# Kernel tuning notes

Measured on AMD Instinct MI355X. Metric: run time of the kernel, lower is better.

## Reference

```python
import jax, jax.numpy as jnp
import numpy as np

N = 50000      # nodes
E = 800000     # edges
D = 128        # hidden_dim == out_dim
VOCAB = 50000  # in_size


def setup_inputs() -> dict:
    key = jax.random.key(0)
    ks = jax.random.split(key, 8)
    batch = jax.random.randint(ks[0], (N,), 0, VOCAB)
    src = jax.random.randint(ks[1], (E,), 0, N)
    dst = jax.random.randint(ks[2], (E,), 0, N)
    emb = jax.random.normal(ks[3], (VOCAB, D), dtype=jnp.float32) * 0.02
    s = 1.0 / np.sqrt(D)
    W1 = jax.random.normal(ks[4], (D, D), dtype=jnp.float32) * s
    W2 = jax.random.normal(ks[5], (D, D), dtype=jnp.float32) * s
    W3 = jax.random.normal(ks[6], (D, D), dtype=jnp.float32) * s
    b1 = jnp.zeros((D,), jnp.float32)
    b2 = jnp.zeros((D,), jnp.float32)
    b3 = jnp.zeros((D,), jnp.float32)
    return {"batch": batch, "src": src, "dst": dst, "emb": emb,
            "W1": W1, "b1": b1, "W2": W2, "b2": b2, "W3": W3, "b3": b3}


def reference(batch, src, dst, emb, W1, b1, W2, b2, W3, b3):
    # embedding lookup over node ids
    x = emb[batch]  # [N, D]
    ones = jnp.ones((E,), x.dtype)
    # DGL GraphConv norm='both': symmetric normalization, degrees clamped >= 1
    deg_out = jnp.clip(jax.ops.segment_sum(ones, src, num_segments=N), 1.0)
    deg_in = jnp.clip(jax.ops.segment_sum(ones, dst, num_segments=N), 1.0)
    norm_src = deg_out ** -0.5  # [N]
    norm_dst = deg_in ** -0.5   # [N]

    def gcn_layer(h, W, b):
        m = (h * norm_src[:, None])[src]                       # gather src messages [E, D]
        agg = jax.ops.segment_sum(m, dst, num_segments=N)      # SpMM aggregate [N, D]
        agg = agg * norm_dst[:, None]
        # dropout p=0.0 is identity; activation is ReLU
        return jax.nn.relu(agg @ W + b)

    x = gcn_layer(x, W1, b1)
    x = gcn_layer(x, W2, b2)
    x = gcn_layer(x, W3, b3)
    return x
```

## Files before the change

### kernel.cpp

```cpp
#include <hip/hip_runtime.h>
#include <math.h>

typedef float f4 __attribute__((ext_vector_type(4)));
typedef float f32x4 __attribute__((ext_vector_type(4)));
typedef short s8 __attribute__((ext_vector_type(8)));
typedef short s4 __attribute__((ext_vector_type(4)));

static constexpr int N = 50000;
static constexpr int E = 800000;
static constexpr int D = 128;
static constexpr int SCAN_NB = (N + 255) / 256;
static constexpr int MBLK = 128;
static constexpr int GRID_M = (N + MBLK - 1) / MBLK;
static constexpr int N_PAD = GRID_M * MBLK;
static constexpr int WT_PITCH = 136;

__device__ inline unsigned short f32_bf16_rne(float x) {
    unsigned u = __float_as_uint(x);
    return (unsigned short)((u + 0x7FFF + ((u >> 16) & 1)) >> 16);
}
__device__ inline float bf16_f32(unsigned short h) {
    return __uint_as_float((unsigned)h << 16);
}

__global__ void deg_kernel(const int* __restrict__ src, const int* __restrict__ dst,
                           int* __restrict__ deg_out, int* __restrict__ deg_in) {
    int e = blockIdx.x * 256 + threadIdx.x;
    if (e < E) {
        atomicAdd(&deg_out[src[e]], 1);
        atomicAdd(&deg_in[dst[e]], 1);
    }
}

__global__ __launch_bounds__(256) void scan_bsum_norm_kernel(
    const int* __restrict__ deg_out, const int* __restrict__ deg_in,
    float* __restrict__ norm_src, float* __restrict__ norm_dst,
    int* __restrict__ bsums) {
    int i = blockIdx.x * 256 + threadIdx.x;
    int v = 0;
    if (i < N) {
        norm_src[i] = rsqrtf(fmaxf((float)deg_out[i], 1.0f));
        norm_dst[i] = rsqrtf(fmaxf((float)deg_in[i], 1.0f));
        v = deg_in[i];
    }
#pragma unroll
    for (int off = 1; off < 64; off <<= 1) v += __shfl_xor(v, off, 64);
    __shared__ int ws[4];
    if ((threadIdx.x & 63) == 0) ws[threadIdx.x >> 6] = v;
    __syncthreads();
    if (threadIdx.x == 0) bsums[blockIdx.x] = ws[0] + ws[1] + ws[2] + ws[3];
}

__global__ __launch_bounds__(256) void scan_final_kernel(const int* __restrict__ deg,
                                                         const int* __restrict__ bsums,
                                                         int* __restrict__ row_ptr) {
    __shared__ int s[256];
    __shared__ int base_s;
    int b = blockIdx.x, t = threadIdx.x;

    int bv = (t < b && t < SCAN_NB) ? bsums[t] : 0;
#pragma unroll
    for (int off = 1; off < 64; off <<= 1) bv += __shfl_xor(bv, off, 64);
    __shared__ int wsb[4];
    if ((t & 63) == 0) wsb[t >> 6] = bv;
    __syncthreads();
    if (t == 0) base_s = wsb[0] + wsb[1] + wsb[2] + wsb[3];

    int i = b * 256 + t;
    s[t] = (i < N) ? deg[i] : 0;
    __syncthreads();
    for (int off = 1; off < 256; off <<= 1) {
        int v = (t >= off) ? s[t - off] : 0;
        __syncthreads();
        s[t] += v;
        __syncthreads();
    }
    if (i < N) row_ptr[i + 1] = s[t] + base_s;
    if (i == 0) row_ptr[0] = 0;
}

__global__ void fill_kernel(const int* __restrict__ src, const int* __restrict__ dst,
                            const int* __restrict__ row_ptr, int* __restrict__ cursor,
                            unsigned short* __restrict__ csr_src) {
    int e = blockIdx.x * 256 + threadIdx.x;
    if (e < E) {
        int d = dst[e];
        int pos = row_ptr[d] + atomicAdd(&cursor[d], 1);
        csr_src[pos] = (unsigned short)src[e];
    }
}

__global__ void gather_kernel(const int* __restrict__ batch, const float* __restrict__ emb,
                              const float* __restrict__ norm_src, float* __restrict__ hs) {
    int gid = blockIdx.x * 256 + threadIdx.x;
    int i = gid >> 5;
    int c = (gid & 31) << 2;
    if (i < N) {
        float s = norm_src[i];
        f4 v = *(const f4*)(emb + (size_t)batch[i] * D + c);
        *(f4*)(hs + (size_t)i * D + c) = v * s;
    }
}

__global__ void agg_kernel(const int* __restrict__ row_ptr,
                           const unsigned short* __restrict__ csr_src,
                           const float* __restrict__ hs,
                           short* __restrict__ agg_h, short* __restrict__ agg_l) {
    int gid = blockIdx.x * 256 + threadIdx.x;
    int node = gid >> 6;
    if (node >= N) return;
    int lane = threadIdx.x & 63;
    int grp = lane >> 5;
    int col = (lane & 31) << 2;
    int beg = row_ptr[node], end = row_ptr[node + 1];

    f4 a0 = (f4)0.0f, a1 = (f4)0.0f, a2 = (f4)0.0f, a3 = (f4)0.0f;
    f4 a4 = (f4)0.0f, a5 = (f4)0.0f, a6 = (f4)0.0f, a7 = (f4)0.0f;
    int e = beg + grp;
    for (; e + 14 < end; e += 16) {
        int s0 = csr_src[e];
        int s1 = csr_src[e + 2];
        int s2 = csr_src[e + 4];
        int s3 = csr_src[e + 6];
        int s4 = csr_src[e + 8];
        int s5 = csr_src[e + 10];
        int s6 = csr_src[e + 12];
        int s7 = csr_src[e + 14];
        a0 += *(const f4*)(hs + (size_t)s0 * D + col);
        a1 += *(const f4*)(hs + (size_t)s1 * D + col);
        a2 += *(const f4*)(hs + (size_t)s2 * D + col);
        a3 += *(const f4*)(hs + (size_t)s3 * D + col);
        a4 += *(const f4*)(hs + (size_t)s4 * D + col);
        a5 += *(const f4*)(hs + (size_t)s5 * D + col);
        a6 += *(const f4*)(hs + (size_t)s6 * D + col);
        a7 += *(const f4*)(hs + (size_t)s7 * D + col);
    }
    for (; e < end; e += 2)
        a0 += *(const f4*)(hs + (size_t)csr_src[e] * D + col);
    a0 += a1; a2 += a3; a4 += a5; a6 += a7;
    a0 += a2; a4 += a6;
    a0 += a4;

    f4 o;
#pragma unroll
    for (int j = 0; j < 4; ++j)
        o[j] = a0[j] + __shfl_xor(a0[j], 32, 64);
    if (grp == 0) {
        s4 oh, ol;
#pragma unroll
        for (int j = 0; j < 4; ++j) {
            unsigned short h = f32_bf16_rne(o[j]);
            oh[j] = (short)h;
            ol[j] = (short)f32_bf16_rne(o[j] - bf16_f32(h));
        }
        *(s4*)(agg_h + (size_t)node * D + col) = oh;
        *(s4*)(agg_l + (size_t)node * D + col) = ol;
    }
}

__global__ void wprep_kernel(const float* __restrict__ W1, const float* __restrict__ W2,
                             const float* __restrict__ W3, short* __restrict__ wt) {
    int idx = blockIdx.x * 256 + threadIdx.x;
    if (idx >= 3 * D * D) return;
    int l = idx >> 14;
    int e = idx & (D * D - 1);
    int n = e >> 7, k = e & 127;
    const float* W = (l == 0) ? W1 : ((l == 1) ? W2 : W3);
    float w = W[(size_t)k * D + n];
    unsigned short h = f32_bf16_rne(w);
    unsigned short lo = f32_bf16_rne(w - bf16_f32(h));
    wt[(size_t)l * 2 * D * D + (size_t)n * D + k] = (short)h;
    wt[(size_t)l * 2 * D * D + D * D + (size_t)n * D + k] = (short)lo;
}

__global__ __launch_bounds__(512, 2) void gemm_mfma_kernel(
    const short* __restrict__ Ah, const short* __restrict__ Al,
    const short* __restrict__ wth,
    const float* __restrict__ bias, const float* __restrict__ norm_dst,
    const float* __restrict__ post, float* __restrict__ out) {
    __shared__ short wt_h[D * WT_PITCH];
    __shared__ short wt_l[D * WT_PITCH];

    int tid = threadIdx.x;
    const short* gh = wth;
    const short* gl = wth + (size_t)D * D;

#pragma unroll
    for (int it = 0; it < 4; ++it) {
        int c = tid + it * 512;
        int n = c >> 4, kc = c & 15;
        *(s8*)(&wt_h[n * WT_PITCH + kc * 8]) = *(const s8*)(gh + (size_t)n * D + kc * 8);
        *(s8*)(&wt_l[n * WT_PITCH + kc * 8]) = *(const s8*)(gl + (size_t)n * D + kc * 8);
    }
    __syncthreads();

    int wv = tid >> 6;
    int lane = tid & 63;
    int lg = lane >> 4;
    int lr = lane & 15;

    int arow = blockIdx.x * MBLK + wv * 16 + lr;
    const short* ahp = Ah + (size_t)arow * D;
    const short* alp = Al + (size_t)arow * D;

    f32x4 acc[8];
#pragma unroll
    for (int nt = 0; nt < 8; ++nt) acc[nt] = (f32x4)0.0f;

#pragma unroll
    for (int kt = 0; kt < 4; ++kt) {
        int ko = kt * 32 + lg * 8;
        s8 ah = *(const s8*)(ahp + ko);
        s8 al = *(const s8*)(alp + ko);
#pragma unroll
        for (int nt = 0; nt < 8; ++nt) {
            int bidx = (nt * 16 + lr) * WT_PITCH + ko;
            s8 bh = *(const s8*)(&wt_h[bidx]);
            s8 bl = *(const s8*)(&wt_l[bidx]);
            acc[nt] = __builtin_amdgcn_mfma_f32_16x16x32_bf16(ah, bh, acc[nt], 0, 0, 0);
            acc[nt] = __builtin_amdgcn_mfma_f32_16x16x32_bf16(al, bh, acc[nt], 0, 0, 0);
            acc[nt] = __builtin_amdgcn_mfma_f32_16x16x32_bf16(ah, bl, acc[nt], 0, 0, 0);
        }
    }

    int r0 = blockIdx.x * MBLK + wv * 16 + lg * 4;
    float nd[4], ps[4];
#pragma unroll
    for (int i = 0; i < 4; ++i) {
        int gr = r0 + i;
        nd[i] = (gr < N) ? norm_dst[gr] : 0.0f;
        ps[i] = (gr < N) ? (post ? post[gr] : 1.0f) : 0.0f;
    }
#pragma unroll
    for (int nt = 0; nt < 8; ++nt) {
        int col = nt * 16 + lr;
        float bv = bias[col];
#pragma unroll
        for (int i = 0; i < 4; ++i) {
            int gr = r0 + i;
            if (gr < N) {
                float v = fmaxf(acc[nt][i] * nd[i] + bv, 0.0f) * ps[i];
                out[(size_t)gr * D + col] = v;
            }
        }
    }
}

extern "C" void kernel_launch(void* const* d_in, const int* in_sizes, int n_in,
                              void* d_out, int out_size, void* d_ws, size_t ws_size,
                              hipStream_t stream) {
    const int*   batch = (const int*)d_in[0];
    const int*   src   = (const int*)d_in[1];
    const int*   dst   = (const int*)d_in[2];
    const float* emb   = (const float*)d_in[3];
    const float* W1    = (const float*)d_in[4];
    const float* b1    = (const float*)d_in[5];
    const float* W2    = (const float*)d_in[6];
    const float* b2    = (const float*)d_in[7];
    const float* W3    = (const float*)d_in[8];
    const float* b3    = (const float*)d_in[9];
    float* out = (float*)d_out;

    float*          norm_src = (float*)d_ws;
    float*          norm_dst = norm_src + N;
    int*            row_ptr  = (int*)(norm_dst + N);
    unsigned short* csr_src  = (unsigned short*)(row_ptr + (N + 1));
    float*          hs       = (float*)(csr_src + E) + 2;
    short*          agg_h    = (short*)(hs + (size_t)N_PAD * D);
    short*          agg_l    = agg_h + (size_t)N_PAD * D;
    short*          wt       = agg_l + (size_t)N_PAD * D;
    int*            deg_out  = (int*)agg_h;
    int*            deg_in   = deg_out + N;
    int*            cursor   = deg_in + N;
    int*            bsums    = cursor + N;

    hipMemsetAsync(deg_out, 0, 3 * (size_t)N * sizeof(int), stream);
    deg_kernel<<<(E + 255) / 256, 256, 0, stream>>>(src, dst, deg_out, deg_in);
    scan_bsum_norm_kernel<<<SCAN_NB, 256, 0, stream>>>(deg_out, deg_in,
                                                       norm_src, norm_dst, bsums);
    scan_final_kernel<<<SCAN_NB, 256, 0, stream>>>(deg_in, bsums, row_ptr);
    fill_kernel<<<(E + 255) / 256, 256, 0, stream>>>(src, dst, row_ptr, cursor,
                                                     csr_src);
    gather_kernel<<<((size_t)N * 32 + 255) / 256, 256, 0, stream>>>(batch, emb,
                                                                    norm_src, hs);
    wprep_kernel<<<(3 * D * D + 255) / 256, 256, 0, stream>>>(W1, W2, W3, wt);

    const float* bs[3] = {b1, b2, b3};
    for (int l = 0; l < 3; ++l) {
        bool last = (l == 2);
        agg_kernel<<<((size_t)N * 64 + 255) / 256, 256, 0, stream>>>(
            row_ptr, csr_src, hs, agg_h, agg_l);
        gemm_mfma_kernel<<<GRID_M, 512, 0, stream>>>(
            agg_h, agg_l, wt + (size_t)l * 2 * D * D, bs[l], norm_dst,
            last ? nullptr : norm_src,
            last ? out : hs);
    }
}
```

Before: 378.1 us.

## Slice features into column blocks and aggregate per slice with XCC-affine work queues

Stores node features and aggregated outputs in 16 column slices of 8 floats each, so every gather for a slice reads from a 1.6MB working set that can stay in cache. The aggregation kernel becomes persistent: blocks pull 256-node chunks from per-slice atomic queues, and each XCC starts on a different slice to improve L2 locality. Each thread now handles a whole node for one slice, which replaces the wavefront-per-node scheme. The cost is 16 passes over the CSR indices, load imbalance between threads that have different degrees, and a GEMM that now reads A and writes hs in the strided slice layout.

```diff
diff --git a/kernel.cpp b/kernel.cpp
--- a/kernel.cpp
+++ b/kernel.cpp
@@ -1,10 +1,10 @@
 #include <hip/hip_runtime.h>
 #include <math.h>
+#include <stdint.h>
 
 typedef float f4 __attribute__((ext_vector_type(4)));
 typedef float f32x4 __attribute__((ext_vector_type(4)));
 typedef short s8 __attribute__((ext_vector_type(8)));
-typedef short s4 __attribute__((ext_vector_type(4)));
 
 static constexpr int N = 50000;
 static constexpr int E = 800000;
@@ -14,6 +14,10 @@
 static constexpr int GRID_M = (N + MBLK - 1) / MBLK;
 static constexpr int N_PAD = GRID_M * MBLK;
 static constexpr int WT_PITCH = 136;
+static constexpr int NSLICE = 16;
+static constexpr size_t SL = (size_t)N_PAD * 8;
+static constexpr int AGG_BLOCKS = 1024;
+static constexpr int CHUNK = 256;
 
 __device__ inline unsigned short f32_bf16_rne(float x) {
     unsigned u = __float_as_uint(x);
@@ -91,70 +95,15 @@
 }
 
 __global__ void gather_kernel(const int* __restrict__ batch, const float* __restrict__ emb,
-                              const float* __restrict__ norm_src, float* __restrict__ hs) {
+                              const float* __restrict__ norm_src, float* __restrict__ hs_t) {
     int gid = blockIdx.x * 256 + threadIdx.x;
     int i = gid >> 5;
     int c = (gid & 31) << 2;
     if (i < N) {
         float s = norm_src[i];
         f4 v = *(const f4*)(emb + (size_t)batch[i] * D + c);
-        *(f4*)(hs + (size_t)i * D + c) = v * s;
-    }
-}
-
-__global__ void agg_kernel(const int* __restrict__ row_ptr,
-                           const unsigned short* __restrict__ csr_src,
-                           const float* __restrict__ hs,
-                           short* __restrict__ agg_h, short* __restrict__ agg_l) {
-    int gid = blockIdx.x * 256 + threadIdx.x;
-    int node = gid >> 6;
-    if (node >= N) return;
-    int lane = threadIdx.x & 63;
-    int grp = lane >> 5;
-    int col = (lane & 31) << 2;
-    int beg = row_ptr[node], end = row_ptr[node + 1];
-
-    f4 a0 = (f4)0.0f, a1 = (f4)0.0f, a2 = (f4)0.0f, a3 = (f4)0.0f;
-    f4 a4 = (f4)0.0f, a5 = (f4)0.0f, a6 = (f4)0.0f, a7 = (f4)0.0f;
-    int e = beg + grp;
-    for (; e + 14 < end; e += 16) {
-        int s0 = csr_src[e];
-        int s1 = csr_src[e + 2];
-        int s2 = csr_src[e + 4];
-        int s3 = csr_src[e + 6];
-        int s4 = csr_src[e + 8];
-        int s5 = csr_src[e + 10];
-        int s6 = csr_src[e + 12];
-        int s7 = csr_src[e + 14];
-        a0 += *(const f4*)(hs + (size_t)s0 * D + col);
-        a1 += *(const f4*)(hs + (size_t)s1 * D + col);
-        a2 += *(const f4*)(hs + (size_t)s2 * D + col);
-        a3 += *(const f4*)(hs + (size_t)s3 * D + col);
-        a4 += *(const f4*)(hs + (size_t)s4 * D + col);
-        a5 += *(const f4*)(hs + (size_t)s5 * D + col);
-        a6 += *(const f4*)(hs + (size_t)s6 * D + col);
-        a7 += *(const f4*)(hs + (size_t)s7 * D + col);
-    }
-    for (; e < end; e += 2)
-        a0 += *(const f4*)(hs + (size_t)csr_src[e] * D + col);
-    a0 += a1; a2 += a3; a4 += a5; a6 += a7;
-    a0 += a2; a4 += a6;
-    a0 += a4;
-
-    f4 o;
-#pragma unroll
-    for (int j = 0; j < 4; ++j)
-        o[j] = a0[j] + __shfl_xor(a0[j], 32, 64);
-    if (grp == 0) {
-        s4 oh, ol;
-#pragma unroll
-        for (int j = 0; j < 4; ++j) {
-            unsigned short h = f32_bf16_rne(o[j]);
-            oh[j] = (short)h;
-            ol[j] = (short)f32_bf16_rne(o[j] - bf16_f32(h));
-        }
-        *(s4*)(agg_h + (size_t)node * D + col) = oh;
-        *(s4*)(agg_l + (size_t)node * D + col) = ol;
+        int slice = c >> 3, cc = c & 7;
+        *(f4*)(hs_t + (size_t)slice * SL + (size_t)i * 8 + cc) = v * s;
     }
 }
 
@@ -173,6 +122,71 @@
     wt[(size_t)l * 2 * D * D + D * D + (size_t)n * D + k] = (short)lo;
 }
 
+__global__ __launch_bounds__(256) void agg_kernel(
+    const int* __restrict__ row_ptr, const unsigned short* __restrict__ csr_src,
+    const float* __restrict__ hs_t,
+    short* __restrict__ agg_h_t, short* __restrict__ agg_l_t,
+    int* __restrict__ qcur) {
+    unsigned xcc;
+    asm volatile("s_getreg_b32 %0, hwreg(HW_REG_XCC_ID)" : "=s"(xcc));
+    int tid = threadIdx.x;
+    __shared__ int chunk_s;
+
+    for (int qi = 0; qi < NSLICE; ++qi) {
+        int q = ((xcc << 1) + qi) & (NSLICE - 1);
+        const float* hsq = hs_t + (size_t)q * SL;
+        short* ahq = agg_h_t + (size_t)q * SL;
+        short* alq = agg_l_t + (size_t)q * SL;
+        while (true) {
+            __syncthreads();
+            if (tid == 0) chunk_s = atomicAdd(&qcur[q], CHUNK);
+            __syncthreads();
+            int base = chunk_s;
+            if (base >= N) break;
+            int node = base + tid;
+            if (node < N) {
+                int beg = row_ptr[node], end = row_ptr[node + 1];
+                f4 a0 = (f4)0.0f, a1 = (f4)0.0f, a2 = (f4)0.0f, a3 = (f4)0.0f;
+                f4 b0 = (f4)0.0f, b1 = (f4)0.0f, b2 = (f4)0.0f, b3 = (f4)0.0f;
+                int e = beg;
+                for (; e + 3 < end; e += 4) {
+                    int s0 = csr_src[e];
+                    int s1 = csr_src[e + 1];
+                    int s2 = csr_src[e + 2];
+                    int s3 = csr_src[e + 3];
+                    const f4* p0 = (const f4*)(hsq + (size_t)s0 * 8);
+                    const f4* p1 = (const f4*)(hsq + (size_t)s1 * 8);
+                    const f4* p2 = (const f4*)(hsq + (size_t)s2 * 8);
+                    const f4* p3 = (const f4*)(hsq + (size_t)s3 * 8);
+                    a0 += p0[0]; b0 += p0[1];
+                    a1 += p1[0]; b1 += p1[1];
+                    a2 += p2[0]; b2 += p2[1];
+                    a3 += p3[0]; b3 += p3[1];
+                }
+                for (; e < end; ++e) {
+                    const f4* p0 = (const f4*)(hsq + (size_t)csr_src[e] * 8);
+                    a0 += p0[0]; b0 += p0[1];
+                }
+                a0 += a1; a2 += a3; a0 += a2;
+                b0 += b1; b2 += b3; b0 += b2;
+
+                s8 oh, ol;
+#pragma unroll
+                for (int j = 0; j < 4; ++j) {
+                    unsigned short h = f32_bf16_rne(a0[j]);
+                    oh[j] = (short)h;
+                    ol[j] = (short)f32_bf16_rne(a0[j] - bf16_f32(h));
+                    unsigned short h2 = f32_bf16_rne(b0[j]);
+                    oh[j + 4] = (short)h2;
+                    ol[j + 4] = (short)f32_bf16_rne(b0[j] - bf16_f32(h2));
+                }
+                *(s8*)(ahq + (size_t)node * 8) = oh;
+                *(s8*)(alq + (size_t)node * 8) = ol;
+            }
+        }
+    }
+}
+
 __global__ __launch_bounds__(512, 2) void gemm_mfma_kernel(
     const short* __restrict__ Ah, const short* __restrict__ Al,
     const short* __restrict__ wth,
@@ -200,8 +214,6 @@
     int lr = lane & 15;
 
     int arow = blockIdx.x * MBLK + wv * 16 + lr;
-    const short* ahp = Ah + (size_t)arow * D;
-    const short* alp = Al + (size_t)arow * D;
 
     f32x4 acc[8];
 #pragma unroll
@@ -209,9 +221,10 @@
 
 #pragma unroll
     for (int kt = 0; kt < 4; ++kt) {
+        int slice = kt * 4 + lg;
+        s8 ah = *(const s8*)(Ah + (size_t)slice * SL + (size_t)arow * 8);
+        s8 al = *(const s8*)(Al + (size_t)slice * SL + (size_t)arow * 8);
         int ko = kt * 32 + lg * 8;
-        s8 ah = *(const s8*)(ahp + ko);
-        s8 al = *(const s8*)(alp + ko);
 #pragma unroll
         for (int nt = 0; nt < 8; ++nt) {
             int bidx = (nt * 16 + lr) * WT_PITCH + ko;
@@ -240,7 +253,12 @@
             int gr = r0 + i;
             if (gr < N) {
                 float v = fmaxf(acc[nt][i] * nd[i] + bv, 0.0f) * ps[i];
-                out[(size_t)gr * D + col] = v;
+                if (post) {
+                    int slice = col >> 3, cc = col & 7;
+                    out[(size_t)slice * SL + (size_t)gr * 8 + cc] = v;
+                } else {
+                    out[(size_t)gr * D + col] = v;
+                }
             }
         }
     }
@@ -265,16 +283,18 @@
     float*          norm_dst = norm_src + N;
     int*            row_ptr  = (int*)(norm_dst + N);
     unsigned short* csr_src  = (unsigned short*)(row_ptr + (N + 1));
-    float*          hs       = (float*)(csr_src + E) + 2;
-    short*          agg_h    = (short*)(hs + (size_t)N_PAD * D);
-    short*          agg_l    = agg_h + (size_t)N_PAD * D;
-    short*          wt       = agg_l + (size_t)N_PAD * D;
-    int*            deg_out  = (int*)agg_h;
+    float*          hs_t     = (float*)((((uintptr_t)(csr_src + E)) + 15) & ~(uintptr_t)15);
+    short*          agg_h_t  = (short*)(hs_t + (size_t)NSLICE * SL);
+    short*          agg_l_t  = agg_h_t + (size_t)NSLICE * SL;
+    short*          wt       = agg_l_t + (size_t)NSLICE * SL;
+    int*            qcur     = (int*)(wt + (size_t)3 * 2 * D * D);
+    int*            deg_out  = (int*)agg_h_t;
     int*            deg_in   = deg_out + N;
     int*            cursor   = deg_in + N;
     int*            bsums    = cursor + N;
 
     hipMemsetAsync(deg_out, 0, 3 * (size_t)N * sizeof(int), stream);
+    hipMemsetAsync(qcur, 0, 3 * NSLICE * sizeof(int), stream);
     deg_kernel<<<(E + 255) / 256, 256, 0, stream>>>(src, dst, deg_out, deg_in);
     scan_bsum_norm_kernel<<<SCAN_NB, 256, 0, stream>>>(deg_out, deg_in,
                                                        norm_src, norm_dst, bsums);
@@ -282,17 +302,17 @@
     fill_kernel<<<(E + 255) / 256, 256, 0, stream>>>(src, dst, row_ptr, cursor,
                                                      csr_src);
     gather_kernel<<<((size_t)N * 32 + 255) / 256, 256, 0, stream>>>(batch, emb,
-                                                                    norm_src, hs);
+                                                                    norm_src, hs_t);
     wprep_kernel<<<(3 * D * D + 255) / 256, 256, 0, stream>>>(W1, W2, W3, wt);
 
     const float* bs[3] = {b1, b2, b3};
     for (int l = 0; l < 3; ++l) {
         bool last = (l == 2);
-        agg_kernel<<<((size_t)N * 64 + 255) / 256, 256, 0, stream>>>(
-            row_ptr, csr_src, hs, agg_h, agg_l);
+        agg_kernel<<<AGG_BLOCKS, 256, 0, stream>>>(
+            row_ptr, csr_src, hs_t, agg_h_t, agg_l_t, qcur + l * NSLICE);
         gemm_mfma_kernel<<<GRID_M, 512, 0, stream>>>(
-            agg_h, agg_l, wt + (size_t)l * 2 * D * D, bs[l], norm_dst,
+            agg_h_t, agg_l_t, wt + (size_t)l * 2 * D * D, bs[l], norm_dst,
             last ? nullptr : norm_src,
-            last ? out : hs);
-    }
-}
+            last ? out : hs_t);
+    }
+}
```

After: 853.0 us. +125.6%, slower.

## Replace global-atomic degree count and CSR fill with LDS range-partitioned histograms

Applied to the files above, without the earlier changes.

Degree counting and CSR filling switch from per-edge global atomics to a 16x16 grid of blocks. Each block takes one edge chunk and one node range and keeps LDS histograms for it. Per-chunk partial counts are reduced and prefix-summed per node, which gives deterministic chunk offsets, and the fill kernel then uses LDS atomics for cursors. This removes global atomic contention and the memset. The cost is that each edge is read 16 times, once per range block, and only 256 blocks are launched.

```diff
diff --git a/kernel.cpp b/kernel.cpp
--- a/kernel.cpp
+++ b/kernel.cpp
@@ -14,6 +14,10 @@
 static constexpr int GRID_M = (N + MBLK - 1) / MBLK;
 static constexpr int N_PAD = GRID_M * MBLK;
 static constexpr int WT_PITCH = 136;
+static constexpr int NCH = 16;
+static constexpr int NRG = 16;
+static constexpr int EPC = E / NCH;
+static constexpr int RSZ = N / NRG;
 
 __device__ inline unsigned short f32_bf16_rne(float x) {
     unsigned u = __float_as_uint(x);
@@ -23,26 +27,53 @@
     return __uint_as_float((unsigned)h << 16);
 }
 
-__global__ void deg_kernel(const int* __restrict__ src, const int* __restrict__ dst,
-                           int* __restrict__ deg_out, int* __restrict__ deg_in) {
-    int e = blockIdx.x * 256 + threadIdx.x;
-    if (e < E) {
-        atomicAdd(&deg_out[src[e]], 1);
-        atomicAdd(&deg_in[dst[e]], 1);
-    }
-}
-
-__global__ __launch_bounds__(256) void scan_bsum_norm_kernel(
-    const int* __restrict__ deg_out, const int* __restrict__ deg_in,
+__global__ __launch_bounds__(256) void hist_kernel(
+    const int* __restrict__ src, const int* __restrict__ dst,
+    int* __restrict__ partial_src, int* __restrict__ partial_dst) {
+    __shared__ int hsrc[RSZ];
+    __shared__ int hdst[RSZ];
+    int b = blockIdx.x;
+    int c = b >> 4, r = b & 15;
+    int tid = threadIdx.x;
+    for (int j = tid; j < RSZ; j += 256) { hsrc[j] = 0; hdst[j] = 0; }
+    __syncthreads();
+    int rlo = r * RSZ, rhi = rlo + RSZ;
+    int ebase = c * EPC;
+    for (int e = ebase + tid; e < ebase + EPC; e += 256) {
+        int s = src[e], d = dst[e];
+        if (s >= rlo && s < rhi) atomicAdd(&hsrc[s - rlo], 1);
+        if (d >= rlo && d < rhi) atomicAdd(&hdst[d - rlo], 1);
+    }
+    __syncthreads();
+    for (int j = tid; j < RSZ; j += 256) {
+        partial_src[(size_t)c * N + rlo + j] = hsrc[j];
+        partial_dst[(size_t)c * N + rlo + j] = hdst[j];
+    }
+}
+
+__global__ __launch_bounds__(256) void reduce_norm_kernel(
+    const int* __restrict__ partial_src, int* __restrict__ partial_dst,
     float* __restrict__ norm_src, float* __restrict__ norm_dst,
-    int* __restrict__ bsums) {
+    int* __restrict__ deg_in, int* __restrict__ bsums) {
     int i = blockIdx.x * 256 + threadIdx.x;
-    int v = 0;
+    int din = 0;
     if (i < N) {
-        norm_src[i] = rsqrtf(fmaxf((float)deg_out[i], 1.0f));
-        norm_dst[i] = rsqrtf(fmaxf((float)deg_in[i], 1.0f));
-        v = deg_in[i];
-    }
+        int dout = 0;
+#pragma unroll
+        for (int c = 0; c < NCH; ++c) dout += partial_src[(size_t)c * N + i];
+        int run = 0;
+#pragma unroll
+        for (int c = 0; c < NCH; ++c) {
+            int v = partial_dst[(size_t)c * N + i];
+            partial_dst[(size_t)c * N + i] = run;
+            run += v;
+        }
+        din = run;
+        deg_in[i] = din;
+        norm_src[i] = rsqrtf(fmaxf((float)dout, 1.0f));
+        norm_dst[i] = rsqrtf(fmaxf((float)din, 1.0f));
+    }
+    int v = din;
 #pragma unroll
     for (int off = 1; off < 64; off <<= 1) v += __shfl_xor(v, off, 64);
     __shared__ int ws[4];
@@ -79,14 +110,25 @@
     if (i == 0) row_ptr[0] = 0;
 }
 
-__global__ void fill_kernel(const int* __restrict__ src, const int* __restrict__ dst,
-                            const int* __restrict__ row_ptr, int* __restrict__ cursor,
-                            unsigned short* __restrict__ csr_src) {
-    int e = blockIdx.x * 256 + threadIdx.x;
-    if (e < E) {
-        int d = dst[e];
-        int pos = row_ptr[d] + atomicAdd(&cursor[d], 1);
-        csr_src[pos] = (unsigned short)src[e];
+__global__ __launch_bounds__(256) void fill_kernel(
+    const int* __restrict__ src, const int* __restrict__ dst,
+    const int* __restrict__ row_ptr, const int* __restrict__ pfx_dst,
+    unsigned short* __restrict__ csr_src) {
+    __shared__ int cur[RSZ];
+    int b = blockIdx.x;
+    int c = b >> 4, r = b & 15;
+    int tid = threadIdx.x;
+    for (int j = tid; j < RSZ; j += 256) cur[j] = 0;
+    __syncthreads();
+    int rlo = r * RSZ, rhi = rlo + RSZ;
+    int ebase = c * EPC;
+    for (int e = ebase + tid; e < ebase + EPC; e += 256) {
+        int s = src[e], d = dst[e];
+        if (d >= rlo && d < rhi) {
+            int pos = row_ptr[d] + pfx_dst[(size_t)c * N + d]
+                    + atomicAdd(&cur[d - rlo], 1);
+            csr_src[pos] = (unsigned short)s;
+        }
     }
 }
 
@@ -261,26 +303,25 @@
     const float* b3    = (const float*)d_in[9];
     float* out = (float*)d_out;
 
-    float*          norm_src = (float*)d_ws;
-    float*          norm_dst = norm_src + N;
-    int*            row_ptr  = (int*)(norm_dst + N);
-    unsigned short* csr_src  = (unsigned short*)(row_ptr + (N + 1));
-    float*          hs       = (float*)(csr_src + E) + 2;
-    short*          agg_h    = (short*)(hs + (size_t)N_PAD * D);
-    short*          agg_l    = agg_h + (size_t)N_PAD * D;
-    short*          wt       = agg_l + (size_t)N_PAD * D;
-    int*            deg_out  = (int*)agg_h;
-    int*            deg_in   = deg_out + N;
-    int*            cursor   = deg_in + N;
-    int*            bsums    = cursor + N;
-
-    hipMemsetAsync(deg_out, 0, 3 * (size_t)N * sizeof(int), stream);
-    deg_kernel<<<(E + 255) / 256, 256, 0, stream>>>(src, dst, deg_out, deg_in);
-    scan_bsum_norm_kernel<<<SCAN_NB, 256, 0, stream>>>(deg_out, deg_in,
-                                                       norm_src, norm_dst, bsums);
+    float*          norm_src    = (float*)d_ws;
+    float*          norm_dst    = norm_src + N;
+    int*            row_ptr     = (int*)(norm_dst + N);
+    unsigned short* csr_src     = (unsigned short*)(row_ptr + (N + 1));
+    float*          hs          = (float*)(csr_src + E) + 2;
+    short*          agg_h       = (short*)(hs + (size_t)N_PAD * D);
+    short*          agg_l       = agg_h + (size_t)N_PAD * D;
+    short*          wt          = agg_l + (size_t)N_PAD * D;
+    int*            partial_src = (int*)agg_h;
+    int*            partial_dst = partial_src + (size_t)NCH * N;
+    int*            deg_in      = partial_dst + (size_t)NCH * N;
+    int*            bsums       = deg_in + N;
+
+    hist_kernel<<<NCH * NRG, 256, 0, stream>>>(src, dst, partial_src, partial_dst);
+    reduce_norm_kernel<<<SCAN_NB, 256, 0, stream>>>(partial_src, partial_dst,
+                                                    norm_src, norm_dst, deg_in, bsums);
     scan_final_kernel<<<SCAN_NB, 256, 0, stream>>>(deg_in, bsums, row_ptr);
-    fill_kernel<<<(E + 255) / 256, 256, 0, stream>>>(src, dst, row_ptr, cursor,
-                                                     csr_src);
+    fill_kernel<<<NCH * NRG, 256, 0, stream>>>(src, dst, row_ptr, partial_dst,
+                                               csr_src);
     gather_kernel<<<((size_t)N * 32 + 255) / 256, 256, 0, stream>>>(batch, emb,
                                                                     norm_src, hs);
     wprep_kernel<<<(3 * D * D + 255) / 256, 256, 0, stream>>>(W1, W2, W3, wt);
```

Result: slower. 436.5 us (+15.4%).

## Build CSR with per-block LDS histograms instead of global atomics

Applied to the files above, without the earlier changes.

Replaces global-atomic degree counting and cursor-based CSR fill with per-block shared-memory histograms packed as two 16-bit counters per word, a cross-block reduction, and a per-chunk exclusive prefix so the fill runs with LDS atomics only. This removes heavy contention on global atomics and the memset. In exchange it adds extra kernels and large partial-histogram traffic (64 chunks × N entries per side), and the fill and hist phases use only 64 to 128 blocks, which limits parallelism. CSR order within a row becomes deterministic by chunk.

```diff
diff --git a/kernel.cpp b/kernel.cpp
--- a/kernel.cpp
+++ b/kernel.cpp
@@ -14,6 +14,9 @@
 static constexpr int GRID_M = (N + MBLK - 1) / MBLK;
 static constexpr int N_PAD = GRID_M * MBLK;
 static constexpr int WT_PITCH = 136;
+static constexpr int HG = 64;
+static constexpr int EPB = E / HG;
+static constexpr int PACK = N / 2;
 
 __device__ inline unsigned short f32_bf16_rne(float x) {
     unsigned u = __float_as_uint(x);
@@ -23,32 +26,66 @@
     return __uint_as_float((unsigned)h << 16);
 }
 
-__global__ void deg_kernel(const int* __restrict__ src, const int* __restrict__ dst,
-                           int* __restrict__ deg_out, int* __restrict__ deg_in) {
-    int e = blockIdx.x * 256 + threadIdx.x;
-    if (e < E) {
-        atomicAdd(&deg_out[src[e]], 1);
-        atomicAdd(&deg_in[dst[e]], 1);
-    }
-}
-
-__global__ __launch_bounds__(256) void scan_bsum_norm_kernel(
-    const int* __restrict__ deg_out, const int* __restrict__ deg_in,
+__global__ __launch_bounds__(256) void hist_kernel(
+    const int* __restrict__ src, const int* __restrict__ dst,
+    unsigned* __restrict__ psrc, unsigned* __restrict__ pdst) {
+    __shared__ unsigned h[PACK];
+    int b = blockIdx.x;
+    int tid = threadIdx.x;
+    bool isd = b >= HG;
+    int bb = isd ? b - HG : b;
+    const int* ids = isd ? dst : src;
+    for (int j = tid; j < PACK; j += 256) h[j] = 0;
+    __syncthreads();
+    int ebase = bb * EPB;
+    for (int e = ebase + tid; e < ebase + EPB; e += 256) {
+        int v = ids[e];
+        atomicAdd(&h[v >> 1], 1u << ((v & 1) << 4));
+    }
+    __syncthreads();
+    unsigned* out = (isd ? pdst : psrc) + (size_t)bb * PACK;
+    for (int j = tid; j < PACK; j += 256) out[j] = h[j];
+}
+
+__global__ __launch_bounds__(256) void reduce_norm_kernel(
+    const unsigned* __restrict__ psrc, const unsigned* __restrict__ pdst,
     float* __restrict__ norm_src, float* __restrict__ norm_dst,
-    int* __restrict__ bsums) {
+    int* __restrict__ deg_in, int* __restrict__ bsums) {
     int i = blockIdx.x * 256 + threadIdx.x;
-    int v = 0;
+    int din = 0;
     if (i < N) {
-        norm_src[i] = rsqrtf(fmaxf((float)deg_out[i], 1.0f));
-        norm_dst[i] = rsqrtf(fmaxf((float)deg_in[i], 1.0f));
-        v = deg_in[i];
-    }
+        int sh = (i & 1) << 4;
+        int j = i >> 1;
+        int dout = 0;
+#pragma unroll 8
+        for (int b = 0; b < HG; ++b) {
+            dout += (psrc[(size_t)b * PACK + j] >> sh) & 0xFFFF;
+            din  += (pdst[(size_t)b * PACK + j] >> sh) & 0xFFFF;
+        }
+        deg_in[i] = din;
+        norm_src[i] = rsqrtf(fmaxf((float)dout, 1.0f));
+        norm_dst[i] = rsqrtf(fmaxf((float)din, 1.0f));
+    }
+    int v = din;
 #pragma unroll
     for (int off = 1; off < 64; off <<= 1) v += __shfl_xor(v, off, 64);
     __shared__ int ws[4];
     if ((threadIdx.x & 63) == 0) ws[threadIdx.x >> 6] = v;
     __syncthreads();
     if (threadIdx.x == 0) bsums[blockIdx.x] = ws[0] + ws[1] + ws[2] + ws[3];
+}
+
+__global__ __launch_bounds__(256) void prefix_kernel(unsigned* __restrict__ pdst) {
+    int j = blockIdx.x * 256 + threadIdx.x;
+    if (j >= PACK) return;
+    unsigned run0 = 0, run1 = 0;
+#pragma unroll 8
+    for (int c = 0; c < HG; ++c) {
+        unsigned u = pdst[(size_t)c * PACK + j];
+        pdst[(size_t)c * PACK + j] = run0 | (run1 << 16);
+        run0 += u & 0xFFFF;
+        run1 += u >> 16;
+    }
 }
 
 __global__ __launch_bounds__(256) void scan_final_kernel(const int* __restrict__ deg,
@@ -79,14 +116,23 @@
     if (i == 0) row_ptr[0] = 0;
 }
 
-__global__ void fill_kernel(const int* __restrict__ src, const int* __restrict__ dst,
-                            const int* __restrict__ row_ptr, int* __restrict__ cursor,
-                            unsigned short* __restrict__ csr_src) {
-    int e = blockIdx.x * 256 + threadIdx.x;
-    if (e < E) {
-        int d = dst[e];
-        int pos = row_ptr[d] + atomicAdd(&cursor[d], 1);
-        csr_src[pos] = (unsigned short)src[e];
+__global__ __launch_bounds__(256) void fill_kernel(
+    const int* __restrict__ src, const int* __restrict__ dst,
+    const int* __restrict__ row_ptr, const unsigned* __restrict__ pfx,
+    unsigned short* __restrict__ csr_src) {
+    __shared__ unsigned cur[PACK];
+    int c = blockIdx.x;
+    int tid = threadIdx.x;
+    for (int j = tid; j < PACK; j += 256) cur[j] = 0;
+    __syncthreads();
+    int ebase = c * EPB;
+    for (int e = ebase + tid; e < ebase + EPB; e += 256) {
+        int s = src[e], d = dst[e];
+        int sh = (d & 1) << 4;
+        unsigned old = atomicAdd(&cur[d >> 1], 1u << sh);
+        int my = (old >> sh) & 0xFFFF;
+        int p = (pfx[(size_t)c * PACK + (d >> 1)] >> sh) & 0xFFFF;
+        csr_src[row_ptr[d] + p + my] = (unsigned short)s;
     }
 }
 
@@ -269,18 +315,17 @@
     short*          agg_h    = (short*)(hs + (size_t)N_PAD * D);
     short*          agg_l    = agg_h + (size_t)N_PAD * D;
     short*          wt       = agg_l + (size_t)N_PAD * D;
-    int*            deg_out  = (int*)agg_h;
-    int*            deg_in   = deg_out + N;
-    int*            cursor   = deg_in + N;
-    int*            bsums    = cursor + N;
-
-    hipMemsetAsync(deg_out, 0, 3 * (size_t)N * sizeof(int), stream);
-    deg_kernel<<<(E + 255) / 256, 256, 0, stream>>>(src, dst, deg_out, deg_in);
-    scan_bsum_norm_kernel<<<SCAN_NB, 256, 0, stream>>>(deg_out, deg_in,
-                                                       norm_src, norm_dst, bsums);
+    unsigned*       psrc     = (unsigned*)agg_h;
+    unsigned*       pdst     = psrc + (size_t)HG * PACK;
+    int*            deg_in   = (int*)(pdst + (size_t)HG * PACK);
+    int*            bsums    = deg_in + N;
+
+    hist_kernel<<<2 * HG, 256, 0, stream>>>(src, dst, psrc, pdst);
+    reduce_norm_kernel<<<SCAN_NB, 256, 0, stream>>>(psrc, pdst, norm_src, norm_dst,
+                                                    deg_in, bsums);
+    prefix_kernel<<<(PACK + 255) / 256, 256, 0, stream>>>(pdst);
     scan_final_kernel<<<SCAN_NB, 256, 0, stream>>>(deg_in, bsums, row_ptr);
-    fill_kernel<<<(E + 255) / 256, 256, 0, stream>>>(src, dst, row_ptr, cursor,
-                                                     csr_src);
+    fill_kernel<<<HG, 256, 0, stream>>>(src, dst, row_ptr, pdst, csr_src);
     gather_kernel<<<((size_t)N * 32 + 255) / 256, 256, 0, stream>>>(batch, emb,
                                                                     norm_src, hs);
     wprep_kernel<<<(3 * D * D + 255) / 256, 256, 0, stream>>>(W1, W2, W3, wt);
```

Result: faster. 333.8 us (-11.7%).
